# Performance work log

Hardware: AMD Instinct MI355X
Metric: run time of the kernel (lower is better)

## Reference

```python
import jax, jax.numpy as jnp
import numpy as np

H, KVH, DH = 16, 4, 64
DIM = 1024
SCALE_BASE = 4096  # context_len
EPS = 1e-6


def rmsnorm(x, g):
    return x * jax.lax.rsqrt(jnp.mean(x * x, axis=-1, keepdims=True) + EPS) * g


def rope_tables(n, dh, dtype):
    inv_freq = 1.0 / (10000.0 ** (jnp.arange(0, dh, 2, dtype=jnp.float32) / dh))
    t = jnp.arange(n, dtype=jnp.float32) * (SCALE_BASE / n)
    freqs = t[:, None] * inv_freq[None, :]          # [n, dh/2]
    emb = jnp.concatenate([freqs, freqs], axis=-1)  # [n, dh]
    return jnp.cos(emb).astype(dtype), jnp.sin(emb).astype(dtype)


def apply_rope(x, cos, sin):
    # x: [b, h, n, dh]; cos/sin: [n, dh]
    x1, x2 = jnp.split(x, 2, axis=-1)
    rot = jnp.concatenate([-x2, x1], axis=-1)
    return x * cos + rot * sin


def setup_inputs() -> dict:
    key = jax.random.key(0)
    ks = jax.random.split(key, 12)
    B, N = 1, 2048
    std = 0.02
    inp = {
        "x": jax.random.normal(ks[0], (B, N, DIM), jnp.float32),
        "a": jax.random.normal(ks[1], (B, N, DIM), jnp.float32),
        "g_x": jnp.ones((DIM,), jnp.float32),
        "g_a": jnp.ones((DIM,), jnp.float32),
        "Wq_x": jax.random.normal(ks[2], (DIM, H * DH), jnp.float32) * std,
        "Wkv_x": jax.random.normal(ks[3], (DIM, 2 * KVH * DH), jnp.float32) * std,
        "Wq_a": jax.random.normal(ks[4], (DIM, H * DH), jnp.float32) * std,
        "Wkv_a": jax.random.normal(ks[5], (DIM, 2 * KVH * DH), jnp.float32) * std,
        "Wout_x": jax.random.normal(ks[6], (H * DH, DIM), jnp.float32) * std,
        "bout_x": jnp.zeros((DIM,), jnp.float32),
        "Wout_a": jax.random.normal(ks[7], (H * DH, DIM), jnp.float32) * std,
        "bout_a": jnp.zeros((DIM,), jnp.float32),
    }
    return inp


def _split_heads(t, h):
    b, n, hd = t.shape
    return t.reshape(b, n, h, hd // h).transpose(0, 2, 1, 3)  # b h n d


def _stream_qkv(s, g, Wq, Wkv):
    s = rmsnorm(s, g)
    q = _split_heads(s @ Wq, H)                 # [b, H, n, DH]
    kv = s @ Wkv
    k, v = jnp.split(kv, 2, axis=-1)
    k = _split_heads(k, KVH)                    # [b, KVH, n, DH]
    v = _split_heads(v, KVH)
    return q, k, v


def reference(x, a, g_x, g_a, Wq_x, Wkv_x, Wq_a, Wkv_a, Wout_x, bout_x, Wout_a, bout_a):
    B, Nx, _ = x.shape
    Na = a.shape[1]
    scale = DH ** -0.5
    r = H // KVH

    q_x, k_x, v_x = _stream_qkv(x, g_x, Wq_x, Wkv_x)
    q_a, k_a, v_a = _stream_qkv(a, g_a, Wq_a, Wkv_a)

    cos_x, sin_x = rope_tables(Nx, DH, x.dtype)
    cos_a, sin_a = rope_tables(Na, DH, a.dtype)
    q_x, k_x = apply_rope(q_x, cos_x, sin_x), apply_rope(k_x, cos_x, sin_x)
    q_a, k_a = apply_rope(q_a, cos_a, sin_a), apply_rope(k_a, cos_a, sin_a)

    # NOTE: original scales q by dim_head**-0.5 AND sdpa scales again -> 1/DH total
    q_x = q_x * scale
    q_a = q_a * scale

    # GQA expansion: einops 'b h n d -> b (r h) n d' == tile heads
    tile = lambda t: jnp.tile(t, (1, r, 1, 1))
    k_x, v_x, k_a, v_a = tile(k_x), tile(v_x), tile(k_a), tile(v_a)

    # pack [a, x] along seq
    q = jnp.concatenate([q_a, q_x], axis=2)
    k = jnp.concatenate([k_a, k_x], axis=2)
    v = jnp.concatenate([v_a, v_x], axis=2)

    scores = jnp.einsum('bhqd,bhkd->bhqk', q, k) * scale  # sdpa's own scale
    attn = jax.nn.softmax(scores, axis=-1)
    out = jnp.einsum('bhqk,bhkd->bhqd', attn, v)          # [b, H, Na+Nx, DH]

    out_a, out_x = out[:, :, :Na], out[:, :, Na:]
    merge = lambda t: t.transpose(0, 2, 1, 3).reshape(B, -1, H * DH)
    out_x = merge(out_x) @ Wout_x + bout_x
    out_a = merge(out_a) @ Wout_a + bout_a
    return out_x, out_a
```

## Files before the change

kernel.cpp:

```cpp
#include <hip/hip_runtime.h>
#include <hip/hip_bf16.h>
#include <stdint.h>
#include <math.h>


#define NSEQ 2048
#define NJ   4096
#define DIMM 1024

typedef __attribute__((ext_vector_type(4))) float f32x4;
typedef __attribute__((ext_vector_type(8))) short bf16x8;
typedef __attribute__((ext_vector_type(4))) short bf16x4;

__device__ __forceinline__ unsigned short f2bf(float f) {
  union { float f; uint32_t u; } v; v.f = f;
  return (unsigned short)((v.u + 0x7FFFu + ((v.u >> 16) & 1u)) >> 16);
}

__device__ __forceinline__ float bf2f(unsigned short h) {
  union { uint32_t u; float f; } v; v.u = ((uint32_t)h) << 16;
  return v.f;
}

__device__ __forceinline__ uint32_t pack2bf(float a, float b) {
  __hip_bfloat162 h = __float22bfloat162_rn(float2{a, b});
  union { __hip_bfloat162 h; uint32_t u; } c; c.h = h;
  return c.u;
}

#if defined(__has_builtin)
#if __has_builtin(__builtin_amdgcn_exp2f)
#define FAST_EXP2(x) __builtin_amdgcn_exp2f(x)
#endif
#endif
#ifndef FAST_EXP2
#define FAST_EXP2(x) exp2f(x)
#endif

__device__ __forceinline__ void glds16(const void* g, void* l) {
  __builtin_amdgcn_global_load_lds(
      (const __attribute__((address_space(1))) unsigned int*)g,
      (__attribute__((address_space(3))) unsigned int*)l, 16, 0, 0);
}

__global__ __launch_bounds__(256) void prep_kernel(
    const float* __restrict__ xa, const float* __restrict__ xx,
    const float* __restrict__ ga, const float* __restrict__ gx,
    const float* __restrict__ wqa, const float* __restrict__ wqx,
    const float* __restrict__ wkva, const float* __restrict__ wkvx,
    const float* __restrict__ woa, const float* __restrict__ wox,
    unsigned short* __restrict__ XN, unsigned short* __restrict__ WQT,
    unsigned short* __restrict__ WKVT, unsigned short* __restrict__ WOT,
    float* __restrict__ cosT, float* __restrict__ sinT) {
  __shared__ float tile[32][33];
  __shared__ float red[4];
  int bid = blockIdx.x, t = threadIdx.x;
  if (bid < 256) {
    int idx = bid * 256 + t;
    int pos = idx >> 5, i = idx & 31;
    double inv = pow(10000.0, -(double)i / 32.0);
    double ang = (double)(2 * pos) * inv;
    cosT[idx] = (float)cos(ang);
    sinT[idx] = (float)sin(ang);
  } else if (bid < 6400) {
    int b = bid - 256;
    int z = b >> 10, yx = b & 1023;
    int n0 = (yx >> 5) * 32, k0 = (yx & 31) * 32;
    int s = z & 1, ty = z >> 1;
    int N = (ty == 1) ? 512 : 1024;
    if (n0 >= N) return;
    const float* src = (z == 0) ? wqa : (z == 1) ? wqx : (z == 2) ? wkva
                     : (z == 3) ? wkvx : (z == 4) ? woa : wox;
    unsigned short* dst = (ty == 0) ? WQT + (size_t)s * 1024 * 1024
                        : (ty == 1) ? WKVT + (size_t)s * 512 * 1024
                                    : WOT + (size_t)s * 1024 * 1024;
    int r = t >> 3, c4 = (t & 7) * 4;
    f32x4 v = *(const f32x4*)(src + (size_t)(k0 + r) * N + n0 + c4);
    tile[r][c4 + 0] = v.x; tile[r][c4 + 1] = v.y;
    tile[r][c4 + 2] = v.z; tile[r][c4 + 3] = v.w;
    __syncthreads();
    int nn = t >> 3, kk = (t & 7) * 4;
    bf16x4 o;
    o.x = (short)f2bf(tile[kk + 0][nn]);
    o.y = (short)f2bf(tile[kk + 1][nn]);
    o.z = (short)f2bf(tile[kk + 2][nn]);
    o.w = (short)f2bf(tile[kk + 3][nn]);
    *(bf16x4*)(dst + (size_t)(n0 + nn) * 1024 + k0 + kk) = o;
  } else {
    int b = bid - 6400;
    int s = b >> 11, row = b & 2047;
    const float* src = (s == 0 ? xa : xx) + (size_t)row * DIMM;
    const float* g = (s == 0 ? ga : gx);
    f32x4 v = *(const f32x4*)(src + t * 4);
    float ss = v.x * v.x + v.y * v.y + v.z * v.z + v.w * v.w;
#pragma unroll
    for (int o = 32; o > 0; o >>= 1) ss += __shfl_xor(ss, o, 64);
    if ((t & 63) == 0) red[t >> 6] = ss;
    __syncthreads();
    float tot = red[0] + red[1] + red[2] + red[3];
    float rs = rsqrtf(tot * (1.0f / DIMM) + 1e-6f);
    f32x4 gv = *(const f32x4*)(g + t * 4);
    bf16x4 o;
    o.x = (short)f2bf(v.x * rs * gv.x);
    o.y = (short)f2bf(v.y * rs * gv.y);
    o.z = (short)f2bf(v.z * rs * gv.z);
    o.w = (short)f2bf(v.w * rs * gv.w);
    *(bf16x4*)(XN + ((size_t)s * NSEQ + row) * DIMM + t * 4) = o;
  }
}

__device__ __forceinline__ void gemm128_mainloop(
    const unsigned short* __restrict__ Ag, const unsigned short* __restrict__ Bg,
    unsigned short* As, unsigned short* Bs, f32x4 acc[4][4]) {
  int t = threadIdx.x;
  int lane = t & 63, wid = t >> 6;
  int wm = (wid >> 1) * 64, wn = (wid & 1) * 64;
  int l15 = lane & 15, quad = lane >> 4;
  int srow = t >> 2, sko = (t & 3) * 8;
  const unsigned short* ga = Ag + (size_t)srow * 1024 + sko;
  const unsigned short* gb = Bg + (size_t)srow * 1024 + sko;
  unsigned short* la = As + t * 8;
  unsigned short* lb = Bs + t * 8;
#pragma unroll
  for (int mi = 0; mi < 4; ++mi)
#pragma unroll
    for (int j = 0; j < 4; ++j) acc[mi][j] = (f32x4){0.f, 0.f, 0.f, 0.f};
  for (int kt = 0; kt < 32; ++kt) {
    int k0 = kt * 32;
    __syncthreads();
    glds16(ga + k0, la);
    glds16(ga + 64 * 1024 + k0, la + 2048);
    glds16(gb + k0, lb);
    glds16(gb + 64 * 1024 + k0, lb + 2048);
    __syncthreads();
    bf16x8 af[4], bfr[4];
#pragma unroll
    for (int mi = 0; mi < 4; ++mi)
      af[mi] = *(const bf16x8*)(As + (wm + mi * 16 + l15) * 32 + quad * 8);
#pragma unroll
    for (int j = 0; j < 4; ++j)
      bfr[j] = *(const bf16x8*)(Bs + (wn + j * 16 + l15) * 32 + quad * 8);
#pragma unroll
    for (int mi = 0; mi < 4; ++mi)
#pragma unroll
      for (int j = 0; j < 4; ++j)
        acc[mi][j] = __builtin_amdgcn_mfma_f32_16x16x32_bf16(af[mi], bfr[j],
                                                             acc[mi][j], 0, 0, 0);
  }
}

__global__ __launch_bounds__(256) void gemm_qkv_kernel(
    const unsigned short* __restrict__ XN, const unsigned short* __restrict__ WQT,
    const unsigned short* __restrict__ WKVT, const float* __restrict__ cosT,
    const float* __restrict__ sinT, unsigned short* __restrict__ QB,
    unsigned short* __restrict__ KB, unsigned short* __restrict__ VTMP) {
  __shared__ unsigned short As[128 * 32], Bs[128 * 32];
  int n0 = blockIdx.x * 128, m0 = blockIdx.y * 128;
  int s = (m0 >= 2048) ? 1 : 0;
  const unsigned short* Ag = XN + (size_t)m0 * 1024;
  const unsigned short* Bg = (n0 < 1024)
      ? WQT + (size_t)s * 1024 * 1024 + (size_t)n0 * 1024
      : WKVT + (size_t)s * 512 * 1024 + (size_t)(n0 - 1024) * 1024;
  f32x4 acc[4][4];
  gemm128_mainloop(Ag, Bg, As, Bs, acc);
  int t = threadIdx.x, lane = t & 63, wid = t >> 6;
  int wm = (wid >> 1) * 64, wn = (wid & 1) * 64;
  int l15 = lane & 15, quad = lane >> 4;
  int coln = n0 + wn;
  if (coln < 1280) {
    bool isq = coln < 1024;
    float sc = isq ? (1.4426950408889634f / 64.0f) : 1.0f;
    unsigned short* dstBase;
    if (isq) dstBase = QB + (size_t)(coln >> 6) * NJ * 64;
    else     dstBase = KB + (size_t)((coln - 1024) >> 6) * NJ * 64;
#pragma unroll
    for (int mi = 0; mi < 4; ++mi)
#pragma unroll
      for (int r = 0; r < 4; ++r) {
        int jr = m0 + wm + mi * 16 + quad * 4 + r;
        int pos = jr & 2047;
#pragma unroll
        for (int jp = 0; jp < 2; ++jp) {
          int i = jp * 16 + l15;
          float c = cosT[pos * 32 + i], sn = sinT[pos * 32 + i];
          float x1 = acc[mi][jp][r], x2 = acc[mi][jp + 2][r];
          dstBase[(size_t)jr * 64 + jp * 16 + l15]      = f2bf((x1 * c - x2 * sn) * sc);
          dstBase[(size_t)jr * 64 + 32 + jp * 16 + l15] = f2bf((x2 * c + x1 * sn) * sc);
        }
      }
  } else {
    int cvb = coln - 1280;
#pragma unroll
    for (int mi = 0; mi < 4; ++mi)
#pragma unroll
      for (int j = 0; j < 4; ++j)
#pragma unroll
        for (int r = 0; r < 4; ++r) {
          int jr = m0 + wm + mi * 16 + quad * 4 + r;
          VTMP[(size_t)jr * 256 + cvb + j * 16 + l15] = f2bf(acc[mi][j][r]);
        }
  }
}

__global__ __launch_bounds__(256) void vtrans_kernel(
    const unsigned short* __restrict__ VTMP, unsigned short* __restrict__ VT) {
  __shared__ unsigned short tile[32][40];
  int r0 = blockIdx.x * 32, c0 = blockIdx.y * 32;
  int t = threadIdx.x;
  int r = t >> 3, c4 = (t & 7) * 4;
  bf16x4 v = *(const bf16x4*)(VTMP + (size_t)(r0 + r) * 256 + c0 + c4);
  tile[r][c4 + 0] = (unsigned short)v.x; tile[r][c4 + 1] = (unsigned short)v.y;
  tile[r][c4 + 2] = (unsigned short)v.z; tile[r][c4 + 3] = (unsigned short)v.w;
  __syncthreads();
  int nn = t >> 3, kk = (t & 7) * 4;
  bf16x4 o;
  o.x = (short)tile[kk + 0][nn]; o.y = (short)tile[kk + 1][nn];
  o.z = (short)tile[kk + 2][nn]; o.w = (short)tile[kk + 3][nn];
  *(bf16x4*)(VT + (size_t)(c0 + nn) * NJ + r0 + kk) = o;
}

__global__ __launch_bounds__(256, 3) void attn_kernel(
    const unsigned short* __restrict__ QB, const unsigned short* __restrict__ KB,
    const unsigned short* __restrict__ VT, unsigned short* __restrict__ OP,
    float* __restrict__ LS) {
  __shared__ unsigned short Ks[2][64 * 72];
  __shared__ unsigned short Vs[2][64 * 72];
  int h = blockIdx.y, qt = blockIdx.x, z = blockIdx.z;
  int hk = h & 3;
  int t = threadIdx.x, lane = t & 63, w = t >> 6;
  int l15 = lane & 15, quad = lane >> 4;
  int q0 = qt * 128 + w * 16;
  bf16x8 qf[2][2];
#pragma unroll
  for (int mi = 0; mi < 2; ++mi) {
    const unsigned short* qp = QB + ((size_t)h * NJ + q0 + mi * 64 + l15) * 64;
    qf[mi][0] = *(const bf16x8*)(qp + quad * 8);
    qf[mi][1] = *(const bf16x8*)(qp + 32 + quad * 8);
  }
  f32x4 oT[2][4];
  f32x4 oL[2];
#pragma unroll
  for (int mi = 0; mi < 2; ++mi) {
    oL[mi] = (f32x4){0.f, 0.f, 0.f, 0.f};
#pragma unroll
    for (int db = 0; db < 4; ++db) oT[mi][db] = (f32x4){0.f, 0.f, 0.f, 0.f};
  }
  bf16x4 vone;
  {
    short one = (short)0x3F80;
    short v = (l15 == 0) ? one : (short)0;
    vone = (bf16x4){v, v, v, v};
  }
  const unsigned short* Kg = KB + ((size_t)hk * NJ + (size_t)z * 2048) * 64;
  const unsigned short* Vg = VT + (size_t)hk * 64 * NJ + z * 2048;
  int ky = t >> 3, dof = (t & 7) * 8;
  const unsigned short* KgA = Kg + (size_t)ky * 64 + dof;
  const unsigned short* KgB = Kg + (size_t)(32 + ky) * 64 + dof;
  const unsigned short* VgA = Vg + (size_t)ky * NJ + dof;
  const unsigned short* VgB = Vg + (size_t)(32 + ky) * NJ + dof;
  bf16x8 kr0 = *(const bf16x8*)(KgA);
  bf16x8 kr1 = *(const bf16x8*)(KgB);
  bf16x8 vr0 = *(const bf16x8*)(VgA);
  bf16x8 vr1 = *(const bf16x8*)(VgB);
  *(bf16x8*)(Ks[0] + ky * 72 + dof) = kr0;
  *(bf16x8*)(Ks[0] + (32 + ky) * 72 + dof) = kr1;
  *(bf16x8*)(Vs[0] + ky * 72 + dof) = vr0;
  *(bf16x8*)(Vs[0] + (32 + ky) * 72 + dof) = vr1;
  kr0 = *(const bf16x8*)(KgA + 4096);
  kr1 = *(const bf16x8*)(KgB + 4096);
  vr0 = *(const bf16x8*)(VgA + 64);
  vr1 = *(const bf16x8*)(VgB + 64);
  __syncthreads();
  for (int kt = 0; kt < 32; ++kt) {
    int cur = kt & 1;
    unsigned short* Kd = Ks[cur ^ 1];
    unsigned short* Vd = Vs[cur ^ 1];
    *(bf16x8*)(Kd + ky * 72 + dof) = kr0;
    *(bf16x8*)(Kd + (32 + ky) * 72 + dof) = kr1;
    *(bf16x8*)(Vd + ky * 72 + dof) = vr0;
    *(bf16x8*)(Vd + (32 + ky) * 72 + dof) = vr1;
    int tn = (kt + 2) & 31;
    kr0 = *(const bf16x8*)(KgA + (size_t)tn * 4096);
    kr1 = *(const bf16x8*)(KgB + (size_t)tn * 4096);
    vr0 = *(const bf16x8*)(VgA + tn * 64);
    vr1 = *(const bf16x8*)(VgB + tn * 64);
    const unsigned short* Kc = Ks[cur];
    const unsigned short* Vc = Vs[cur];
    f32x4 sx[2][4];
#pragma unroll
    for (int jb = 0; jb < 4; ++jb) {
      const unsigned short* kp = Kc + (jb * 16 + l15) * 72;
      bf16x8 kf0 = *(const bf16x8*)(kp + quad * 8);
      bf16x8 kf1 = *(const bf16x8*)(kp + 32 + quad * 8);
      f32x4 z0 = (f32x4){0.f, 0.f, 0.f, 0.f};
      z0 = __builtin_amdgcn_mfma_f32_16x16x32_bf16(kf0, qf[0][0], z0, 0, 0, 0);
      z0 = __builtin_amdgcn_mfma_f32_16x16x32_bf16(kf1, qf[0][1], z0, 0, 0, 0);
      sx[0][jb] = z0;
      f32x4 z1 = (f32x4){0.f, 0.f, 0.f, 0.f};
      z1 = __builtin_amdgcn_mfma_f32_16x16x32_bf16(kf0, qf[1][0], z1, 0, 0, 0);
      z1 = __builtin_amdgcn_mfma_f32_16x16x32_bf16(kf1, qf[1][1], z1, 0, 0, 0);
      sx[1][jb] = z1;
    }
    bf16x4 pb[2][4];
#pragma unroll
    for (int mi = 0; mi < 2; ++mi)
#pragma unroll
      for (int jb = 0; jb < 4; ++jb) {
        float p0 = FAST_EXP2(sx[mi][jb][0]);
        float p1 = FAST_EXP2(sx[mi][jb][1]);
        float p2 = FAST_EXP2(sx[mi][jb][2]);
        float p3 = FAST_EXP2(sx[mi][jb][3]);
        union { bf16x4 v; uint32_t u[2]; } pk;
        pk.u[0] = pack2bf(p0, p1);
        pk.u[1] = pack2bf(p2, p3);
        pb[mi][jb] = pk.v;
      }
#pragma unroll
    for (int db = 0; db < 4; ++db)
#pragma unroll
      for (int jb = 0; jb < 4; ++jb) {
        bf16x4 va = *(const bf16x4*)(Vc + (db * 16 + l15) * 72 + jb * 16 + quad * 4);
        oT[0][db] = __builtin_amdgcn_mfma_f32_16x16x16bf16_1k(va, pb[0][jb],
                                                              oT[0][db], 0, 0, 0);
        oT[1][db] = __builtin_amdgcn_mfma_f32_16x16x16bf16_1k(va, pb[1][jb],
                                                              oT[1][db], 0, 0, 0);
      }
#pragma unroll
    for (int mi = 0; mi < 2; ++mi)
#pragma unroll
      for (int jb = 0; jb < 4; ++jb)
        oL[mi] = __builtin_amdgcn_mfma_f32_16x16x16bf16_1k(vone, pb[mi][jb],
                                                           oL[mi], 0, 0, 0);
    __syncthreads();
  }
#pragma unroll
  for (int mi = 0; mi < 2; ++mi) {
    float s = oL[mi][0];
    s += __shfl_xor(s, 16, 64);
    s += __shfl_xor(s, 32, 64);
    int qrow = q0 + mi * 64 + l15;
    if (quad == 0) LS[((size_t)z * 16 + h) * NJ + qrow] = s;
#pragma unroll
    for (int db = 0; db < 4; ++db) {
      union { bf16x4 v; uint32_t u[2]; } ov;
      ov.u[0] = pack2bf(oT[mi][db][0], oT[mi][db][1]);
      ov.u[1] = pack2bf(oT[mi][db][2], oT[mi][db][3]);
      *(bf16x4*)(OP + ((size_t)z * NJ + qrow) * DIMM + h * 64 + db * 16 + quad * 4) = ov.v;
    }
  }
}

__global__ __launch_bounds__(256) void combine_kernel(
    const unsigned short* __restrict__ OP, const float* __restrict__ LS,
    unsigned short* __restrict__ AT) {
  int idx = blockIdx.x * 256 + threadIdx.x;
  int q = idx >> 8;
  int c4 = (idx & 255) * 4;
  int h = c4 >> 6;
  float inv = 1.0f / (LS[(size_t)h * NJ + q] + LS[(size_t)(16 + h) * NJ + q]);
  bf16x4 p0 = *(const bf16x4*)(OP + (size_t)q * DIMM + c4);
  bf16x4 p1 = *(const bf16x4*)(OP + ((size_t)NJ + q) * DIMM + c4);
  bf16x4 o;
#pragma unroll
  for (int i = 0; i < 4; ++i) {
    float a = bf2f((unsigned short)p0[i]) + bf2f((unsigned short)p1[i]);
    o[i] = (short)f2bf(a * inv);
  }
  *(bf16x4*)(AT + (size_t)q * DIMM + c4) = o;
}

__global__ __launch_bounds__(256) void gemm_out_kernel(
    const unsigned short* __restrict__ AT, const unsigned short* __restrict__ WOT,
    const float* __restrict__ ba, const float* __restrict__ bx,
    float* __restrict__ out) {
  __shared__ unsigned short As[128 * 32], Bs[128 * 32];
  int n0 = blockIdx.x * 128, m0 = blockIdx.y * 128;
  int s = (m0 >= 2048) ? 1 : 0;
  const unsigned short* Ag = AT + (size_t)m0 * 1024;
  const unsigned short* Bg = WOT + (size_t)s * 1024 * 1024 + (size_t)n0 * 1024;
  f32x4 acc[4][4];
  gemm128_mainloop(Ag, Bg, As, Bs, acc);
  int t = threadIdx.x, lane = t & 63, wid = t >> 6;
  int wm = (wid >> 1) * 64, wn = (wid & 1) * 64;
  int l15 = lane & 15, quad = lane >> 4;
  const float* bias = s ? bx : ba;
  float* obase = s ? (out + (size_t)(m0 - 2048) * 1024)
                   : (out + (size_t)2048 * 1024 + (size_t)m0 * 1024);
#pragma unroll
  for (int mi = 0; mi < 4; ++mi)
#pragma unroll
    for (int r = 0; r < 4; ++r) {
      int row = wm + mi * 16 + quad * 4 + r;
#pragma unroll
      for (int j = 0; j < 4; ++j) {
        int col = n0 + wn + j * 16 + l15;
        obase[(size_t)row * 1024 + col] = acc[mi][j][r] + bias[col];
      }
    }
}

extern "C" void kernel_launch(void* const* d_in, const int* in_sizes, int n_in,
                              void* d_out, int out_size, void* d_ws, size_t ws_size,
                              hipStream_t stream) {
  const float* x      = (const float*)d_in[0];
  const float* a      = (const float*)d_in[1];
  const float* g_x    = (const float*)d_in[2];
  const float* g_a    = (const float*)d_in[3];
  const float* Wq_x   = (const float*)d_in[4];
  const float* Wkv_x  = (const float*)d_in[5];
  const float* Wq_a   = (const float*)d_in[6];
  const float* Wkv_a  = (const float*)d_in[7];
  const float* Wout_x = (const float*)d_in[8];
  const float* bout_x = (const float*)d_in[9];
  const float* Wout_a = (const float*)d_in[10];
  const float* bout_a = (const float*)d_in[11];
  float* out = (float*)d_out;

  char* ws = (char*)d_ws;
  const size_t MB = 1024 * 1024;
  unsigned short* OP   = (unsigned short*)(ws);
  unsigned short* XN   = (unsigned short*)(ws);
  unsigned short* WQT  = (unsigned short*)(ws + 8 * MB);
  unsigned short* WKVT = (unsigned short*)(ws + 12 * MB);
  unsigned short* VTMP = (unsigned short*)(ws + 14 * MB);
  float* cosT          = (float*)(ws + 16 * MB);
  float* sinT          = (float*)(ws + 16 * MB + 262144);
  unsigned short* WOT  = (unsigned short*)(ws + 17 * MB);
  unsigned short* QB   = (unsigned short*)(ws + 21 * MB);
  unsigned short* KB   = (unsigned short*)(ws + 29 * MB);
  unsigned short* VT   = (unsigned short*)(ws + 31 * MB);
  float* LS            = (float*)(ws + 33 * MB);
  unsigned short* AT   = (unsigned short*)(ws + 34 * MB);

  prep_kernel<<<dim3(10496), dim3(256), 0, stream>>>(
      a, x, g_a, g_x, Wq_a, Wq_x, Wkv_a, Wkv_x, Wout_a, Wout_x,
      XN, WQT, WKVT, WOT, cosT, sinT);
  gemm_qkv_kernel<<<dim3(12, 32), dim3(256), 0, stream>>>(
      XN, WQT, WKVT, cosT, sinT, QB, KB, VTMP);
  vtrans_kernel<<<dim3(128, 8), dim3(256), 0, stream>>>(VTMP, VT);
  attn_kernel<<<dim3(32, 16, 2), dim3(256), 0, stream>>>(QB, KB, VT, OP, LS);
  combine_kernel<<<dim3(4096), dim3(256), 0, stream>>>(OP, LS, AT);
  gemm_out_kernel<<<dim3(8, 32), dim3(256), 0, stream>>>(
      AT, WOT, bout_a, bout_x, out);
}
```

Measured before the change: 245.5 us.

## Fuse V transpose into QKV GEMM and drop split-K attention with combine

The QKV GEMM epilogue now writes V directly in transposed layout, which removes the separate transpose kernel and its temporary buffer. Attention no longer splits the key range across two z-blocks. Each block walks all 64 key tiles and normalizes its output in place, so the partial-sum buffers and the combine kernel are gone. The PV product switches to 16x16x32 MFMA with a permuted K row order and LDS padding of 76, and occupancy is raised to 4 blocks per SM. The cost is half as many attention blocks, each running twice as long, so parallelism drops, and the transposed V writes are strided.

```diff
diff --git a/kernel.cpp b/kernel.cpp
--- a/kernel.cpp
+++ b/kernel.cpp
@@ -7,6 +7,7 @@
 #define NSEQ 2048
 #define NJ   4096
 #define DIMM 1024
+#define LPAD 76
 
 typedef __attribute__((ext_vector_type(4))) float f32x4;
 typedef __attribute__((ext_vector_type(8))) short bf16x8;
@@ -15,11 +16,6 @@
 __device__ __forceinline__ unsigned short f2bf(float f) {
   union { float f; uint32_t u; } v; v.f = f;
   return (unsigned short)((v.u + 0x7FFFu + ((v.u >> 16) & 1u)) >> 16);
-}
-
-__device__ __forceinline__ float bf2f(unsigned short h) {
-  union { uint32_t u; float f; } v; v.u = ((uint32_t)h) << 16;
-  return v.f;
 }
 
 __device__ __forceinline__ uint32_t pack2bf(float a, float b) {
@@ -153,7 +149,7 @@
     const unsigned short* __restrict__ XN, const unsigned short* __restrict__ WQT,
     const unsigned short* __restrict__ WKVT, const float* __restrict__ cosT,
     const float* __restrict__ sinT, unsigned short* __restrict__ QB,
-    unsigned short* __restrict__ KB, unsigned short* __restrict__ VTMP) {
+    unsigned short* __restrict__ KB, unsigned short* __restrict__ VT) {
   __shared__ unsigned short As[128 * 32], Bs[128 * 32];
   int n0 = blockIdx.x * 128, m0 = blockIdx.y * 128;
   int s = (m0 >= 2048) ? 1 : 0;
@@ -193,43 +189,28 @@
 #pragma unroll
     for (int mi = 0; mi < 4; ++mi)
 #pragma unroll
-      for (int j = 0; j < 4; ++j)
-#pragma unroll
-        for (int r = 0; r < 4; ++r) {
-          int jr = m0 + wm + mi * 16 + quad * 4 + r;
-          VTMP[(size_t)jr * 256 + cvb + j * 16 + l15] = f2bf(acc[mi][j][r]);
-        }
-  }
-}
-
-__global__ __launch_bounds__(256) void vtrans_kernel(
-    const unsigned short* __restrict__ VTMP, unsigned short* __restrict__ VT) {
-  __shared__ unsigned short tile[32][40];
-  int r0 = blockIdx.x * 32, c0 = blockIdx.y * 32;
-  int t = threadIdx.x;
-  int r = t >> 3, c4 = (t & 7) * 4;
-  bf16x4 v = *(const bf16x4*)(VTMP + (size_t)(r0 + r) * 256 + c0 + c4);
-  tile[r][c4 + 0] = (unsigned short)v.x; tile[r][c4 + 1] = (unsigned short)v.y;
-  tile[r][c4 + 2] = (unsigned short)v.z; tile[r][c4 + 3] = (unsigned short)v.w;
-  __syncthreads();
-  int nn = t >> 3, kk = (t & 7) * 4;
-  bf16x4 o;
-  o.x = (short)tile[kk + 0][nn]; o.y = (short)tile[kk + 1][nn];
-  o.z = (short)tile[kk + 2][nn]; o.w = (short)tile[kk + 3][nn];
-  *(bf16x4*)(VT + (size_t)(c0 + nn) * NJ + r0 + kk) = o;
-}
-
-__global__ __launch_bounds__(256, 3) void attn_kernel(
+      for (int j = 0; j < 4; ++j) {
+        int d = cvb + j * 16 + l15;
+        int jr0 = m0 + wm + mi * 16 + quad * 4;
+        union { bf16x4 v; uint32_t u[2]; } pv;
+        pv.u[0] = pack2bf(acc[mi][j][0], acc[mi][j][1]);
+        pv.u[1] = pack2bf(acc[mi][j][2], acc[mi][j][3]);
+        *(bf16x4*)(VT + (size_t)d * NJ + jr0) = pv.v;
+      }
+  }
+}
+
+__global__ __launch_bounds__(256, 4) void attn_kernel(
     const unsigned short* __restrict__ QB, const unsigned short* __restrict__ KB,
-    const unsigned short* __restrict__ VT, unsigned short* __restrict__ OP,
-    float* __restrict__ LS) {
-  __shared__ unsigned short Ks[2][64 * 72];
-  __shared__ unsigned short Vs[2][64 * 72];
-  int h = blockIdx.y, qt = blockIdx.x, z = blockIdx.z;
+    const unsigned short* __restrict__ VT, unsigned short* __restrict__ AT) {
+  __shared__ unsigned short Ks[2][64 * LPAD];
+  __shared__ unsigned short Vs[2][64 * LPAD];
+  int h = blockIdx.y, qt = blockIdx.x;
   int hk = h & 3;
   int t = threadIdx.x, lane = t & 63, w = t >> 6;
   int l15 = lane & 15, quad = lane >> 4;
   int q0 = qt * 128 + w * 16;
+  int pl = ((l15 >> 2) << 3) + (l15 & 3);
   bf16x8 qf[2][2];
 #pragma unroll
   for (int mi = 0; mi < 2; ++mi) {
@@ -245,14 +226,13 @@
 #pragma unroll
     for (int db = 0; db < 4; ++db) oT[mi][db] = (f32x4){0.f, 0.f, 0.f, 0.f};
   }
-  bf16x4 vone;
+  bf16x8 vone;
   {
-    short one = (short)0x3F80;
-    short v = (l15 == 0) ? one : (short)0;
-    vone = (bf16x4){v, v, v, v};
-  }
-  const unsigned short* Kg = KB + ((size_t)hk * NJ + (size_t)z * 2048) * 64;
-  const unsigned short* Vg = VT + (size_t)hk * 64 * NJ + z * 2048;
+    short one = (l15 == 0) ? (short)0x3F80 : (short)0;
+    vone = (bf16x8){one, one, one, one, one, one, one, one};
+  }
+  const unsigned short* Kg = KB + (size_t)hk * NJ * 64;
+  const unsigned short* Vg = VT + (size_t)hk * 64 * NJ;
   int ky = t >> 3, dof = (t & 7) * 8;
   const unsigned short* KgA = Kg + (size_t)ky * 64 + dof;
   const unsigned short* KgB = Kg + (size_t)(32 + ky) * 64 + dof;
@@ -262,24 +242,24 @@
   bf16x8 kr1 = *(const bf16x8*)(KgB);
   bf16x8 vr0 = *(const bf16x8*)(VgA);
   bf16x8 vr1 = *(const bf16x8*)(VgB);
-  *(bf16x8*)(Ks[0] + ky * 72 + dof) = kr0;
-  *(bf16x8*)(Ks[0] + (32 + ky) * 72 + dof) = kr1;
-  *(bf16x8*)(Vs[0] + ky * 72 + dof) = vr0;
-  *(bf16x8*)(Vs[0] + (32 + ky) * 72 + dof) = vr1;
+  *(bf16x8*)(Ks[0] + ky * LPAD + dof) = kr0;
+  *(bf16x8*)(Ks[0] + (32 + ky) * LPAD + dof) = kr1;
+  *(bf16x8*)(Vs[0] + ky * LPAD + dof) = vr0;
+  *(bf16x8*)(Vs[0] + (32 + ky) * LPAD + dof) = vr1;
   kr0 = *(const bf16x8*)(KgA + 4096);
   kr1 = *(const bf16x8*)(KgB + 4096);
   vr0 = *(const bf16x8*)(VgA + 64);
   vr1 = *(const bf16x8*)(VgB + 64);
   __syncthreads();
-  for (int kt = 0; kt < 32; ++kt) {
+  for (int kt = 0; kt < 64; ++kt) {
     int cur = kt & 1;
     unsigned short* Kd = Ks[cur ^ 1];
     unsigned short* Vd = Vs[cur ^ 1];
-    *(bf16x8*)(Kd + ky * 72 + dof) = kr0;
-    *(bf16x8*)(Kd + (32 + ky) * 72 + dof) = kr1;
-    *(bf16x8*)(Vd + ky * 72 + dof) = vr0;
-    *(bf16x8*)(Vd + (32 + ky) * 72 + dof) = vr1;
-    int tn = (kt + 2) & 31;
+    *(bf16x8*)(Kd + ky * LPAD + dof) = kr0;
+    *(bf16x8*)(Kd + (32 + ky) * LPAD + dof) = kr1;
+    *(bf16x8*)(Vd + ky * LPAD + dof) = vr0;
+    *(bf16x8*)(Vd + (32 + ky) * LPAD + dof) = vr1;
+    int tn = (kt + 2) & 63;
     kr0 = *(const bf16x8*)(KgA + (size_t)tn * 4096);
     kr1 = *(const bf16x8*)(KgB + (size_t)tn * 4096);
     vr0 = *(const bf16x8*)(VgA + tn * 64);
@@ -289,7 +269,8 @@
     f32x4 sx[2][4];
 #pragma unroll
     for (int jb = 0; jb < 4; ++jb) {
-      const unsigned short* kp = Kc + (jb * 16 + l15) * 72;
+      int row = ((jb >> 1) << 5) + ((jb & 1) << 2) + pl;
+      const unsigned short* kp = Kc + row * LPAD;
       bf16x8 kf0 = *(const bf16x8*)(kp + quad * 8);
       bf16x8 kf1 = *(const bf16x8*)(kp + 32 + quad * 8);
       f32x4 z0 = (f32x4){0.f, 0.f, 0.f, 0.f};
@@ -301,36 +282,34 @@
       z1 = __builtin_amdgcn_mfma_f32_16x16x32_bf16(kf1, qf[1][1], z1, 0, 0, 0);
       sx[1][jb] = z1;
     }
-    bf16x4 pb[2][4];
+    bf16x8 pb[2][2];
 #pragma unroll
     for (int mi = 0; mi < 2; ++mi)
 #pragma unroll
-      for (int jb = 0; jb < 4; ++jb) {
-        float p0 = FAST_EXP2(sx[mi][jb][0]);
-        float p1 = FAST_EXP2(sx[mi][jb][1]);
-        float p2 = FAST_EXP2(sx[mi][jb][2]);
-        float p3 = FAST_EXP2(sx[mi][jb][3]);
-        union { bf16x4 v; uint32_t u[2]; } pk;
-        pk.u[0] = pack2bf(p0, p1);
-        pk.u[1] = pack2bf(p2, p3);
-        pb[mi][jb] = pk.v;
+      for (int sb = 0; sb < 2; ++sb) {
+        union { bf16x8 v; uint32_t u[4]; } pk;
+        pk.u[0] = pack2bf(FAST_EXP2(sx[mi][2 * sb][0]), FAST_EXP2(sx[mi][2 * sb][1]));
+        pk.u[1] = pack2bf(FAST_EXP2(sx[mi][2 * sb][2]), FAST_EXP2(sx[mi][2 * sb][3]));
+        pk.u[2] = pack2bf(FAST_EXP2(sx[mi][2 * sb + 1][0]), FAST_EXP2(sx[mi][2 * sb + 1][1]));
+        pk.u[3] = pack2bf(FAST_EXP2(sx[mi][2 * sb + 1][2]), FAST_EXP2(sx[mi][2 * sb + 1][3]));
+        pb[mi][sb] = pk.v;
       }
 #pragma unroll
     for (int db = 0; db < 4; ++db)
 #pragma unroll
-      for (int jb = 0; jb < 4; ++jb) {
-        bf16x4 va = *(const bf16x4*)(Vc + (db * 16 + l15) * 72 + jb * 16 + quad * 4);
-        oT[0][db] = __builtin_amdgcn_mfma_f32_16x16x16bf16_1k(va, pb[0][jb],
-                                                              oT[0][db], 0, 0, 0);
-        oT[1][db] = __builtin_amdgcn_mfma_f32_16x16x16bf16_1k(va, pb[1][jb],
-                                                              oT[1][db], 0, 0, 0);
+      for (int sb = 0; sb < 2; ++sb) {
+        bf16x8 va = *(const bf16x8*)(Vc + (db * 16 + l15) * LPAD + sb * 32 + quad * 8);
+        oT[0][db] = __builtin_amdgcn_mfma_f32_16x16x32_bf16(va, pb[0][sb],
+                                                            oT[0][db], 0, 0, 0);
+        oT[1][db] = __builtin_amdgcn_mfma_f32_16x16x32_bf16(va, pb[1][sb],
+                                                            oT[1][db], 0, 0, 0);
       }
 #pragma unroll
     for (int mi = 0; mi < 2; ++mi)
 #pragma unroll
-      for (int jb = 0; jb < 4; ++jb)
-        oL[mi] = __builtin_amdgcn_mfma_f32_16x16x16bf16_1k(vone, pb[mi][jb],
-                                                           oL[mi], 0, 0, 0);
+      for (int sb = 0; sb < 2; ++sb)
+        oL[mi] = __builtin_amdgcn_mfma_f32_16x16x32_bf16(vone, pb[mi][sb],
+                                                         oL[mi], 0, 0, 0);
     __syncthreads();
   }
 #pragma unroll
@@ -338,35 +317,16 @@
     float s = oL[mi][0];
     s += __shfl_xor(s, 16, 64);
     s += __shfl_xor(s, 32, 64);
+    float inv = 1.0f / s;
     int qrow = q0 + mi * 64 + l15;
-    if (quad == 0) LS[((size_t)z * 16 + h) * NJ + qrow] = s;
 #pragma unroll
     for (int db = 0; db < 4; ++db) {
       union { bf16x4 v; uint32_t u[2]; } ov;
-      ov.u[0] = pack2bf(oT[mi][db][0], oT[mi][db][1]);
-      ov.u[1] = pack2bf(oT[mi][db][2], oT[mi][db][3]);
-      *(bf16x4*)(OP + ((size_t)z * NJ + qrow) * DIMM + h * 64 + db * 16 + quad * 4) = ov.v;
+      ov.u[0] = pack2bf(oT[mi][db][0] * inv, oT[mi][db][1] * inv);
+      ov.u[1] = pack2bf(oT[mi][db][2] * inv, oT[mi][db][3] * inv);
+      *(bf16x4*)(AT + (size_t)qrow * DIMM + h * 64 + db * 16 + quad * 4) = ov.v;
     }
   }
-}
-
-__global__ __launch_bounds__(256) void combine_kernel(
-    const unsigned short* __restrict__ OP, const float* __restrict__ LS,
-    unsigned short* __restrict__ AT) {
-  int idx = blockIdx.x * 256 + threadIdx.x;
-  int q = idx >> 8;
-  int c4 = (idx & 255) * 4;
-  int h = c4 >> 6;
-  float inv = 1.0f / (LS[(size_t)h * NJ + q] + LS[(size_t)(16 + h) * NJ + q]);
-  bf16x4 p0 = *(const bf16x4*)(OP + (size_t)q * DIMM + c4);
-  bf16x4 p1 = *(const bf16x4*)(OP + ((size_t)NJ + q) * DIMM + c4);
-  bf16x4 o;
-#pragma unroll
-  for (int i = 0; i < 4; ++i) {
-    float a = bf2f((unsigned short)p0[i]) + bf2f((unsigned short)p1[i]);
-    o[i] = (short)f2bf(a * inv);
-  }
-  *(bf16x4*)(AT + (size_t)q * DIMM + c4) = o;
 }
 
 __global__ __launch_bounds__(256) void gemm_out_kernel(
@@ -418,28 +378,23 @@
 
   char* ws = (char*)d_ws;
   const size_t MB = 1024 * 1024;
-  unsigned short* OP   = (unsigned short*)(ws);
   unsigned short* XN   = (unsigned short*)(ws);
   unsigned short* WQT  = (unsigned short*)(ws + 8 * MB);
   unsigned short* WKVT = (unsigned short*)(ws + 12 * MB);
-  unsigned short* VTMP = (unsigned short*)(ws + 14 * MB);
-  float* cosT          = (float*)(ws + 16 * MB);
-  float* sinT          = (float*)(ws + 16 * MB + 262144);
-  unsigned short* WOT  = (unsigned short*)(ws + 17 * MB);
-  unsigned short* QB   = (unsigned short*)(ws + 21 * MB);
-  unsigned short* KB   = (unsigned short*)(ws + 29 * MB);
-  unsigned short* VT   = (unsigned short*)(ws + 31 * MB);
-  float* LS            = (float*)(ws + 33 * MB);
-  unsigned short* AT   = (unsigned short*)(ws + 34 * MB);
+  unsigned short* WOT  = (unsigned short*)(ws + 14 * MB);
+  unsigned short* QB   = (unsigned short*)(ws + 18 * MB);
+  unsigned short* KB   = (unsigned short*)(ws + 26 * MB);
+  unsigned short* VT   = (unsigned short*)(ws + 28 * MB);
+  float* cosT          = (float*)(ws + 30 * MB);
+  float* sinT          = (float*)(ws + 30 * MB + 262144);
+  unsigned short* AT   = XN;
 
   prep_kernel<<<dim3(10496), dim3(256), 0, stream>>>(
       a, x, g_a, g_x, Wq_a, Wq_x, Wkv_a, Wkv_x, Wout_a, Wout_x,
       XN, WQT, WKVT, WOT, cosT, sinT);
   gemm_qkv_kernel<<<dim3(12, 32), dim3(256), 0, stream>>>(
-      XN, WQT, WKVT, cosT, sinT, QB, KB, VTMP);
-  vtrans_kernel<<<dim3(128, 8), dim3(256), 0, stream>>>(VTMP, VT);
-  attn_kernel<<<dim3(32, 16, 2), dim3(256), 0, stream>>>(QB, KB, VT, OP, LS);
-  combine_kernel<<<dim3(4096), dim3(256), 0, stream>>>(OP, LS, AT);
+      XN, WQT, WKVT, cosT, sinT, QB, KB, VT);
+  attn_kernel<<<dim3(32, 16), dim3(256), 0, stream>>>(QB, KB, VT, AT);
   gemm_out_kernel<<<dim3(8, 32), dim3(256), 0, stream>>>(
       AT, WOT, bout_a, bout_x, out);
 }
```

Result: slower. 413.1 us (+68.3%).
